# Kernel tuning notes

Measured on AMD Instinct MI355X. Metric: run time of the kernel, lower is better.

Reference implementation:

```python
import jax, jax.numpy as jnp
import numpy as np

BUCKET_SIZE = 64
N_HASHES = 8
EPS = 1e-6
SELF_MASK_VAL = -1e5


def setup_inputs() -> dict:
    key = jax.random.key(0)
    k1, k2, k3 = jax.random.split(key, 3)
    B, S, D = 8, 4096, 128
    n_buckets = S // BUCKET_SIZE  # 64, even as required
    qk = jax.random.normal(k1, (B, S, D), dtype=jnp.float32)
    v = jax.random.normal(k2, (B, S, D), dtype=jnp.float32)
    # shared random rotations (random_rotations_per_head=False): (dim, n_hashes, n_buckets//2)
    rotations = jax.random.normal(k3, (D, N_HASHES, n_buckets // 2), dtype=jnp.float32)
    return {"qk": qk, "v": v, "rotations": rotations}


def _look_one_back(x):
    # prepend previous chunk (with wraparound) along the key/value axis
    x_extra = jnp.concatenate([x[:, -1:], x[:, :-1]], axis=1)
    return jnp.concatenate([x, x_extra], axis=2)


def reference(qk, v, rotations):
    B, S, D = qk.shape
    n_buckets = S // BUCKET_SIZE
    n_bins = n_buckets
    C = N_HASHES * n_bins  # number of chunks per sequence (chunk size = BUCKET_SIZE)

    # --- hash_vectors ---
    rot = jnp.einsum('btf,fhi->bhti', qk, rotations)          # [B,H,S,nb/2]
    rot = jnp.concatenate([rot, -rot], axis=-1)               # [B,H,S,nb]
    buckets = jnp.argmax(rot, axis=-1)                        # [B,H,S]
    offsets = (jnp.arange(N_HASHES) * n_buckets).reshape(1, -1, 1)
    buckets = (buckets + offsets).reshape(B, -1)              # [B, H*S]

    # --- sort tokens by (bucket, position) ---
    ticker = jnp.arange(N_HASHES * S)[None, :]
    buckets_and_t = S * buckets + (ticker % S)                # unique keys
    sticker = jnp.argsort(buckets_and_t, axis=-1)             # [B, H*S]
    undo_sort = jnpp_argsort = jnp.argsort(sticker, axis=-1)
    st = sticker % S

    sqk = jnp.take_along_axis(qk, st[..., None], axis=1)      # [B,H*S,D]
    sv = jnp.take_along_axis(v, st[..., None], axis=1)

    bq_t = st.reshape(B, C, -1)                               # [B,C,chunk]
    bqk = sqk.reshape(B, C, -1, D)
    bv = sv.reshape(B, C, -1, D)

    bq = bqk
    bk = bqk * jax.lax.rsqrt(jnp.sum(bqk * bqk, axis=-1, keepdims=True) + EPS)

    bk = _look_one_back(bk)                                   # [B,C,2*chunk,D]
    bv = _look_one_back(bv)
    bkv_t = _look_one_back(bq_t)

    dots = jnp.einsum('bcie,bcje->bcij', bq, bk) * (D ** -0.5)
    self_mask = bq_t[:, :, :, None] == bkv_t[:, :, None, :]
    dots = jnp.where(self_mask, SELF_MASK_VAL, dots)

    lse = jax.nn.logsumexp(dots, axis=-1, keepdims=True)
    probs = jnp.exp(dots - lse)
    bo = jnp.einsum('bcij,bcje->bcie', probs, bv)             # [B,C,chunk,D]

    so = bo.reshape(B, -1, D)                                 # [B,H*S,D]
    slogits = lse.reshape(B, -1)                              # [B,H*S]

    # unsort
    o = jnp.take_along_axis(so, undo_sort[..., None], axis=1)
    logits = jnp.take_along_axis(slogits, undo_sort, axis=1)

    # combine the n_hashes rounds with softmax over per-round logsumexp
    o = o.reshape(B, N_HASHES, S, D)
    logits = logits.reshape(B, N_HASHES, S, 1)
    w = jnp.exp(logits - jax.nn.logsumexp(logits, axis=1, keepdims=True))
    out = jnp.sum(o * w, axis=1)                              # [B,S,D]
    return out, buckets
```

## Files before the change

### kernel.cpp

```cpp
#include <hip/hip_runtime.h>
#include <hip/hip_bf16.h>

#define BB 8
#define SS 4096
#define DD 128
#define HH 8
#define NBUCK 64
#define CHUNKSZ 64
#define NCHUNK 512
#define HSTOT 32768
#define ROWB 272

typedef __attribute__((ext_vector_type(8))) short short8_t;
typedef __attribute__((ext_vector_type(4))) float f32x4;

static __device__ __forceinline__ unsigned short f2bf(float f) {
    __hip_bfloat16 h = __float2bfloat16(f);
    return *reinterpret_cast<unsigned short*>(&h);
}
static __device__ __forceinline__ unsigned int pk2bf(float lo, float hi) {
    __hip_bfloat162 h = __float22bfloat162_rn(make_float2(lo, hi));
    return *reinterpret_cast<unsigned int*>(&h);
}
static __device__ __forceinline__ float bf2f(unsigned short u) {
    return __uint_as_float(((unsigned int)u) << 16);
}

__global__ __launch_bounds__(256) void hash_kernel(
    const float* __restrict__ qk, const float* __restrict__ rot,
    unsigned char* __restrict__ bucket_ws, float* __restrict__ bucket_out)
{
    const int tid = threadIdx.x;
    const int bid = blockIdx.x;
    const int b   = bid >> 8;
    const int h   = (bid >> 5) & 7;
    const int t0  = (bid & 31) * 128;
    const int tg  = tid >> 3;
    const int jq  = tid & 7;

    const float* qbase = qk + ((size_t)b * SS + t0 + tg * 4) * DD;
    const float* rbase = rot + h * 32 + jq * 4;

    float acc[4][4];
    #pragma unroll
    for (int r = 0; r < 4; ++r)
        #pragma unroll
        for (int j = 0; j < 4; ++j) acc[r][j] = 0.f;

    for (int c = 0; c < 16; ++c) {
        float4 qv[4][2];
        #pragma unroll
        for (int r = 0; r < 4; ++r) {
            qv[r][0] = *reinterpret_cast<const float4*>(qbase + r * DD + c * 8);
            qv[r][1] = *reinterpret_cast<const float4*>(qbase + r * DD + c * 8 + 4);
        }
        float4 rv[8];
        #pragma unroll
        for (int ff = 0; ff < 8; ++ff)
            rv[ff] = *reinterpret_cast<const float4*>(rbase + (size_t)(c * 8 + ff) * (HH * 32));
        #pragma unroll
        for (int ff = 0; ff < 8; ++ff) {
            #pragma unroll
            for (int r = 0; r < 4; ++r) {
                const float4 qh = qv[r][ff >> 2];
                const float qs = (ff & 2) ? ((ff & 1) ? qh.w : qh.z)
                                          : ((ff & 1) ? qh.y : qh.x);
                acc[r][0] = fmaf(qs, rv[ff].x, acc[r][0]);
                acc[r][1] = fmaf(qs, rv[ff].y, acc[r][1]);
                acc[r][2] = fmaf(qs, rv[ff].z, acc[r][2]);
                acc[r][3] = fmaf(qs, rv[ff].w, acc[r][3]);
            }
        }
    }

    const float TAU = 0.01f;
    #pragma unroll
    for (int r = 0; r < 4; ++r) {
        float bv = -3.0e38f; int bi = 0;
        #pragma unroll
        for (int j = 0; j < 4; ++j) {
            float v = acc[r][j];
            if (v > bv) { bv = v; bi = jq * 4 + j; }
        }
        #pragma unroll
        for (int j = 0; j < 4; ++j) {
            float v = -acc[r][j];
            if (v > bv) { bv = v; bi = 32 + jq * 4 + j; }
        }
        #pragma unroll
        for (int off = 1; off < 8; off <<= 1) {
            float ov = __shfl_xor(bv, off);
            int   oi = __shfl_xor(bi, off);
            if (ov > bv || (ov == bv && oi < bi)) { bv = ov; bi = oi; }
        }
        const float thrv = bv - TAU;
        int cnt = 0;
        #pragma unroll
        for (int j = 0; j < 4; ++j) {
            cnt += (acc[r][j]  > thrv) ? 1 : 0;
            cnt += (-acc[r][j] > thrv) ? 1 : 0;
        }
        #pragma unroll
        for (int off = 1; off < 8; off <<= 1) cnt += __shfl_xor(cnt, off);

        const int t = t0 + tg * 4 + r;
        if (cnt > 1) {
            const float* qrow = qk + ((size_t)b * SS + t) * DD;
            double bvd = -1.0e300; int bid2 = 64;
            #pragma unroll
            for (int j = 0; j < 4; ++j) {
                const bool fp = (acc[r][j] > thrv);
                const bool fn = (-acc[r][j] > thrv);
                if (fp || fn) {
                    const float* rcol = rot + h * 32 + jq * 4 + j;
                    double a = 0.0;
                    for (int f = 0; f < DD; ++f)
                        a = fma((double)qrow[f], (double)rcol[(size_t)f * (HH * 32)], a);
                    if (fp &&  a > bvd)                         { bvd = a;  bid2 = jq * 4 + j; }
                    if (fn && (-a > bvd ||
                               (-a == bvd && 32 + jq * 4 + j < bid2))) { bvd = -a; bid2 = 32 + jq * 4 + j; }
                }
            }
            #pragma unroll
            for (int off = 1; off < 8; off <<= 1) {
                double ov = __shfl_xor(bvd, off);
                int    oi = __shfl_xor(bid2, off);
                if (ov > bvd || (ov == bvd && oi < bid2)) { bvd = ov; bid2 = oi; }
            }
            bi = bid2;
        }
        if (jq == 0) {
            const size_t o = ((size_t)b * HH + h) * SS + t;
            bucket_ws[o]  = (unsigned char)bi;
            bucket_out[o] = (float)(bi + h * NBUCK);
        }
    }
}

__global__ __launch_bounds__(256) void sort_kernel(
    const unsigned char* __restrict__ bucket_ws, int* __restrict__ st)
{
    __shared__ unsigned int hist[256 * 65];
    __shared__ unsigned int totals[64];
    const int tid = threadIdx.x;
    const int bh  = blockIdx.x;

    unsigned int* hrow = &hist[tid * 65];
    #pragma unroll
    for (int j = 0; j < 65; ++j) hrow[j] = 0u;

    const uint4 raw = *reinterpret_cast<const uint4*>(bucket_ws + (size_t)bh * SS + tid * 16);
    unsigned int w[4] = {raw.x, raw.y, raw.z, raw.w};

    #pragma unroll
    for (int c = 0; c < 16; ++c) {
        unsigned int bk = (w[c >> 2] >> ((c & 3) * 8)) & 255u;
        hrow[bk] += 1u;
    }
    __syncthreads();

    if (tid < 64) {
        unsigned int run = 0;
        for (int c2 = 0; c2 < 256; ++c2) {
            unsigned int x = hist[c2 * 65 + tid];
            hist[c2 * 65 + tid] = run;
            run += x;
        }
        totals[tid] = run;
    }
    __syncthreads();
    if (tid == 0) {
        unsigned int base = 0;
        for (int k = 0; k < 64; ++k) { unsigned int x = totals[k]; totals[k] = base; base += x; }
    }
    __syncthreads();

    int* dst = st + (size_t)bh * SS;
    #pragma unroll
    for (int c = 0; c < 16; ++c) {
        unsigned int bk = (w[c >> 2] >> ((c & 3) * 8)) & 255u;
        unsigned int pos = totals[bk] + hrow[bk];
        hrow[bk] += 1u;
        dst[pos] = tid * 16 + c;
    }
}

__global__ __launch_bounds__(256, 4) void attn_kernel(
    const float* __restrict__ qk, const float* __restrict__ vv,
    const int* __restrict__ st, float* __restrict__ logits_ws,
    void* __restrict__ o_ws, const int obf16)
{
    __shared__ __align__(16) char smem[36864];
    char*  Kb    = smem;
    char*  Pb    = smem;
    char*  Vt    = smem + 17408;
    int*   tks   = (int*)(smem + 34816);
    float* ninv  = (float*)(smem + 35328);
    float* psums = (float*)(smem + 35840);

    const int tid = threadIdx.x;
    const int bc  = blockIdx.x;
    const int b   = bc >> 9;
    const int c   = bc & 511;
    const int h   = c >> 6;

    if (tid < 128) {
        int src_c = (tid < 64) ? c : ((c == 0) ? (NCHUNK - 1) : (c - 1));
        tks[tid] = st[(size_t)b * HSTOT + (size_t)src_c * CHUNKSZ + (tid & 63)];
    }
    __syncthreads();

    {
        const int row = tid >> 1, half = tid & 1;
        const int t = tks[row];
        const float* srow = qk + ((size_t)b * SS + t) * DD + half * 64;
        char* krow = Kb + (size_t)row * ROWB + half * 128;
        float ss = 0.f;
        #pragma unroll
        for (int i = 0; i < 8; ++i) {
            float4 v0 = *reinterpret_cast<const float4*>(srow + i * 8);
            float4 v1 = *reinterpret_cast<const float4*>(srow + i * 8 + 4);
            ss = fmaf(v0.x, v0.x, ss); ss = fmaf(v0.y, v0.y, ss);
            ss = fmaf(v0.z, v0.z, ss); ss = fmaf(v0.w, v0.w, ss);
            ss = fmaf(v1.x, v1.x, ss); ss = fmaf(v1.y, v1.y, ss);
            ss = fmaf(v1.z, v1.z, ss); ss = fmaf(v1.w, v1.w, ss);
            uint4 pk;
            pk.x = pk2bf(v0.x, v0.y); pk.y = pk2bf(v0.z, v0.w);
            pk.z = pk2bf(v1.x, v1.y); pk.w = pk2bf(v1.z, v1.w);
            *reinterpret_cast<uint4*>(krow + i * 16) = pk;
        }
        psums[tid] = ss;
    }
    __syncthreads();
    if (tid < 128) ninv[tid] = rsqrtf(psums[2 * tid] + psums[2 * tid + 1] + 1e-6f);
    __syncthreads();

    const int w  = tid >> 6;
    const int ln = tid & 63;
    const int cc = ln & 15;
    const int g  = ln >> 4;

    short8_t aq[4];
    #pragma unroll
    for (int ks = 0; ks < 4; ++ks)
        aq[ks] = *reinterpret_cast<const short8_t*>(Kb + (size_t)(16 * w + cc) * ROWB + ks * 64 + g * 16);

    f32x4 acc[8];
    #pragma unroll
    for (int j = 0; j < 8; ++j) {
        acc[j] = (f32x4){0.f, 0.f, 0.f, 0.f};
        #pragma unroll
        for (int ks = 0; ks < 4; ++ks) {
            short8_t bk = *reinterpret_cast<const short8_t*>(Kb + (size_t)(16 * j + cc) * ROWB + ks * 64 + g * 16);
            acc[j] = __builtin_amdgcn_mfma_f32_16x16x32_bf16(aq[ks], bk, acc[j], 0, 0, 0);
        }
    }

    const float SCALE = 0.088388347648318447f;
    float lse[4];
    float pr[8][4];
    #pragma unroll
    for (int jr = 0; jr < 4; ++jr) {
        const int q  = 16 * w + 4 * g + jr;
        const int tq = tks[q];
        float m = -3.0e38f;
        #pragma unroll
        for (int j = 0; j < 8; ++j) {
            const int k = 16 * j + cc;
            float val = acc[j][jr] * (ninv[k] * SCALE);
            if (tks[k] == tq) val = -1e5f;
            pr[j][jr] = val;
            m = fmaxf(m, val);
        }
        #pragma unroll
        for (int off = 1; off < 16; off <<= 1) m = fmaxf(m, __shfl_xor(m, off));
        float ssum = 0.f;
        #pragma unroll
        for (int j = 0; j < 8; ++j) { float ex = expf(pr[j][jr] - m); pr[j][jr] = ex; ssum += ex; }
        #pragma unroll
        for (int off = 1; off < 16; off <<= 1) ssum += __shfl_xor(ssum, off);
        const float inv = 1.0f / ssum;
        #pragma unroll
        for (int j = 0; j < 8; ++j) pr[j][jr] *= inv;
        lse[jr] = m + logf(ssum);
    }

    const int kp = tid & 63;
    const int db = tid >> 6;
    const int tva = tks[2 * kp], tvb = tks[2 * kp + 1];
    const float* vra = vv + ((size_t)b * SS + tva) * DD + db * 16;
    const float* vrb = vv + ((size_t)b * SS + tvb) * DD + db * 16;
    float4 va[4], vbr[4];
    #pragma unroll
    for (int i = 0; i < 4; ++i) {
        va[i]  = *reinterpret_cast<const float4*>(vra + i * 4);
        vbr[i] = *reinterpret_cast<const float4*>(vrb + i * 4);
    }

    __syncthreads();

    #pragma unroll
    for (int jr = 0; jr < 4; ++jr) {
        const int q = 16 * w + 4 * g + jr;
        #pragma unroll
        for (int j = 0; j < 8; ++j)
            *reinterpret_cast<unsigned short*>(Pb + (size_t)q * ROWB + (16 * j + cc) * 2) = f2bf(pr[j][jr]);
    }
    if (cc == 0) {
        #pragma unroll
        for (int jr = 0; jr < 4; ++jr) {
            const int q = 16 * w + 4 * g + jr;
            logits_ws[((size_t)b * HH + h) * SS + tks[q]] = lse[jr];
        }
    }
    {
        const float* fa = reinterpret_cast<const float*>(va);
        const float* fb = reinterpret_cast<const float*>(vbr);
        #pragma unroll
        for (int i = 0; i < 16; ++i) {
            const int dl = db * 16 + i;
            *reinterpret_cast<unsigned int*>(Vt + (size_t)dl * ROWB + kp * 4) = pk2bf(fa[i], fb[i]);
        }
    }
    #pragma unroll
    for (int i = 0; i < 4; ++i) {
        va[i]  = *reinterpret_cast<const float4*>(vra + 64 + i * 4);
        vbr[i] = *reinterpret_cast<const float4*>(vrb + 64 + i * 4);
    }
    __syncthreads();

    short8_t pa[4];
    #pragma unroll
    for (int ks = 0; ks < 4; ++ks)
        pa[ks] = *reinterpret_cast<const short8_t*>(Pb + (size_t)(16 * w + cc) * ROWB + ks * 64 + g * 16);

    f32x4 oacc[8];
    #pragma unroll
    for (int dt = 0; dt < 4; ++dt) {
        oacc[dt] = (f32x4){0.f, 0.f, 0.f, 0.f};
        #pragma unroll
        for (int ks = 0; ks < 4; ++ks) {
            short8_t vb = *reinterpret_cast<const short8_t*>(Vt + (size_t)(16 * dt + cc) * ROWB + ks * 64 + g * 16);
            oacc[dt] = __builtin_amdgcn_mfma_f32_16x16x32_bf16(pa[ks], vb, oacc[dt], 0, 0, 0);
        }
    }
    __syncthreads();

    {
        const float* fa = reinterpret_cast<const float*>(va);
        const float* fb = reinterpret_cast<const float*>(vbr);
        #pragma unroll
        for (int i = 0; i < 16; ++i) {
            const int dl = db * 16 + i;
            *reinterpret_cast<unsigned int*>(Vt + (size_t)dl * ROWB + kp * 4) = pk2bf(fa[i], fb[i]);
        }
    }
    __syncthreads();

    #pragma unroll
    for (int dt = 4; dt < 8; ++dt) {
        oacc[dt] = (f32x4){0.f, 0.f, 0.f, 0.f};
        #pragma unroll
        for (int ks = 0; ks < 4; ++ks) {
            short8_t vb = *reinterpret_cast<const short8_t*>(Vt + (size_t)(16 * (dt - 4) + cc) * ROWB + ks * 64 + g * 16);
            oacc[dt] = __builtin_amdgcn_mfma_f32_16x16x32_bf16(pa[ks], vb, oacc[dt], 0, 0, 0);
        }
    }

    #pragma unroll
    for (int jr = 0; jr < 4; ++jr) {
        const int q = 16 * w + 4 * g + jr;
        const int t = tks[q];
        const size_t base = (((size_t)b * HH + h) * SS + t) * DD + cc;
        if (!obf16) {
            float* op = (float*)o_ws;
            #pragma unroll
            for (int dt = 0; dt < 8; ++dt) op[base + 16 * dt] = oacc[dt][jr];
        } else {
            unsigned short* op = (unsigned short*)o_ws;
            #pragma unroll
            for (int dt = 0; dt < 8; ++dt) op[base + 16 * dt] = f2bf(oacc[dt][jr]);
        }
    }
}

__global__ __launch_bounds__(256) void combine_kernel(
    const float* __restrict__ logits_ws, const void* __restrict__ o_ws,
    float* __restrict__ outp, const int obf16)
{
    const int gid = blockIdx.x * 256 + threadIdx.x;
    const int row = gid >> 5;
    const int seg = gid & 31;
    const int b = row >> 12;
    const int t = row & 4095;

    float l[8];
    float m = -3.0e38f;
    #pragma unroll
    for (int hh = 0; hh < 8; ++hh) {
        l[hh] = logits_ws[((size_t)b * HH + hh) * SS + t];
        m = fmaxf(m, l[hh]);
    }
    float ssum = 0.f;
    #pragma unroll
    for (int hh = 0; hh < 8; ++hh) { l[hh] = expf(l[hh] - m); ssum += l[hh]; }
    const float inv = 1.0f / ssum;

    float a0 = 0.f, a1 = 0.f, a2 = 0.f, a3 = 0.f;
    #pragma unroll
    for (int hh = 0; hh < 8; ++hh) {
        const float wgt = l[hh] * inv;
        const size_t base = (((size_t)b * HH + hh) * SS + t) * DD + seg * 4;
        if (!obf16) {
            float4 ov = *reinterpret_cast<const float4*>((const float*)o_ws + base);
            a0 = fmaf(wgt, ov.x, a0); a1 = fmaf(wgt, ov.y, a1);
            a2 = fmaf(wgt, ov.z, a2); a3 = fmaf(wgt, ov.w, a3);
        } else {
            uint2 u = *reinterpret_cast<const uint2*>((const unsigned short*)o_ws + base);
            a0 = fmaf(wgt, bf2f((unsigned short)(u.x & 0xffffu)), a0);
            a1 = fmaf(wgt, bf2f((unsigned short)(u.x >> 16)), a1);
            a2 = fmaf(wgt, bf2f((unsigned short)(u.y & 0xffffu)), a2);
            a3 = fmaf(wgt, bf2f((unsigned short)(u.y >> 16)), a3);
        }
    }
    *reinterpret_cast<float4*>(outp + ((size_t)b * SS + t) * DD + seg * 4) =
        make_float4(a0, a1, a2, a3);
}

extern "C" void kernel_launch(void* const* d_in, const int* in_sizes, int n_in,
                              void* d_out, int out_size, void* d_ws, size_t ws_size,
                              hipStream_t stream) {
    const float* qk  = (const float*)d_in[0];
    const float* v   = (const float*)d_in[1];
    const float* rot = (const float*)d_in[2];

    float* out        = (float*)d_out;
    float* bucket_out = out + (size_t)BB * SS * DD;

    char* ws = (char*)d_ws;
    int*            st        = (int*)ws;
    unsigned char*  bucket_ws = (unsigned char*)(ws + 1048576);
    float*          logits_ws = (float*)(ws + 1048576 + 262144);
    void*           o_ws      = (void*)(ws + 2359296);

    const int obf16 = 1;

    hipLaunchKernelGGL(hash_kernel,    dim3(2048), dim3(256), 0, stream, qk, rot, bucket_ws, bucket_out);
    hipLaunchKernelGGL(sort_kernel,    dim3(64),   dim3(256), 0, stream, bucket_ws, st);
    hipLaunchKernelGGL(attn_kernel,    dim3(4096), dim3(256), 0, stream, qk, v, st, logits_ws, o_ws, obf16);
    hipLaunchKernelGGL(combine_kernel, dim3(4096), dim3(256), 0, stream, logits_ws, o_ws, out, obf16);
}
```

Before: 190.1 us.

## Compute LSH rotation projections with bf16 MFMA and wider fp64 tie-break fallback

```diff
diff --git a/kernel.cpp b/kernel.cpp
--- a/kernel.cpp
+++ b/kernel.cpp
@@ -13,6 +13,7 @@
 
 typedef __attribute__((ext_vector_type(8))) short short8_t;
 typedef __attribute__((ext_vector_type(4))) float f32x4;
+typedef __attribute__((ext_vector_type(4))) unsigned int u32x4;
 
 static __device__ __forceinline__ unsigned short f2bf(float f) {
     __hip_bfloat16 h = __float2bfloat16(f);
@@ -26,69 +27,89 @@
     return __uint_as_float(((unsigned int)u) << 16);
 }
 
+__global__ __launch_bounds__(256) void rot_transpose_kernel(
+    const float* __restrict__ rot, unsigned short* __restrict__ rotT)
+{
+    const int col = threadIdx.x;
+    for (int f0 = 0; f0 < DD; f0 += 8) {
+        float v[8];
+        #pragma unroll
+        for (int i = 0; i < 8; ++i) v[i] = rot[(size_t)(f0 + i) * 256 + col];
+        uint4 pk;
+        pk.x = pk2bf(v[0], v[1]); pk.y = pk2bf(v[2], v[3]);
+        pk.z = pk2bf(v[4], v[5]); pk.w = pk2bf(v[6], v[7]);
+        *reinterpret_cast<uint4*>(rotT + (size_t)col * DD + f0) = pk;
+    }
+}
+
+__device__ __noinline__ double f64dot_col(const float* __restrict__ qrow,
+                                          const float* __restrict__ rot, int col)
+{
+    double a = 0.0;
+    for (int f = 0; f < DD; ++f)
+        a = fma((double)qrow[f], (double)rot[(size_t)f * 256 + col], a);
+    return a;
+}
+
 __global__ __launch_bounds__(256) void hash_kernel(
     const float* __restrict__ qk, const float* __restrict__ rot,
+    const unsigned short* __restrict__ rotT,
     unsigned char* __restrict__ bucket_ws, float* __restrict__ bucket_out)
 {
     const int tid = threadIdx.x;
     const int bid = blockIdx.x;
-    const int b   = bid >> 8;
-    const int h   = (bid >> 5) & 7;
-    const int t0  = (bid & 31) * 128;
-    const int tg  = tid >> 3;
-    const int jq  = tid & 7;
-
-    const float* qbase = qk + ((size_t)b * SS + t0 + tg * 4) * DD;
-    const float* rbase = rot + h * 32 + jq * 4;
-
-    float acc[4][4];
-    #pragma unroll
-    for (int r = 0; r < 4; ++r)
-        #pragma unroll
-        for (int j = 0; j < 4; ++j) acc[r][j] = 0.f;
-
-    for (int c = 0; c < 16; ++c) {
-        float4 qv[4][2];
-        #pragma unroll
-        for (int r = 0; r < 4; ++r) {
-            qv[r][0] = *reinterpret_cast<const float4*>(qbase + r * DD + c * 8);
-            qv[r][1] = *reinterpret_cast<const float4*>(qbase + r * DD + c * 8 + 4);
-        }
-        float4 rv[8];
-        #pragma unroll
-        for (int ff = 0; ff < 8; ++ff)
-            rv[ff] = *reinterpret_cast<const float4*>(rbase + (size_t)(c * 8 + ff) * (HH * 32));
-        #pragma unroll
-        for (int ff = 0; ff < 8; ++ff) {
+    const int b   = bid >> 6;
+    const int t0  = (bid & 63) * 64;
+    const int w   = tid >> 6;
+    const int ln  = tid & 63;
+    const int cc  = ln & 15;
+    const int g   = ln >> 4;
+    const int tglob = t0 + w * 16 + cc;
+
+    const float* qrow = qk + ((size_t)b * SS + tglob) * DD;
+
+    f32x4 acc[16];
+    #pragma unroll
+    for (int m = 0; m < 16; ++m) acc[m] = (f32x4){0.f, 0.f, 0.f, 0.f};
+
+    #pragma unroll
+    for (int ks = 0; ks < 4; ++ks) {
+        float4 q0 = *reinterpret_cast<const float4*>(qrow + ks * 32 + g * 8);
+        float4 q1 = *reinterpret_cast<const float4*>(qrow + ks * 32 + g * 8 + 4);
+        u32x4 bq;
+        bq.x = pk2bf(q0.x, q0.y); bq.y = pk2bf(q0.z, q0.w);
+        bq.z = pk2bf(q1.x, q1.y); bq.w = pk2bf(q1.z, q1.w);
+        short8_t bfr = __builtin_bit_cast(short8_t, bq);
+        #pragma unroll
+        for (int m = 0; m < 16; ++m) {
+            short8_t af = *reinterpret_cast<const short8_t*>(
+                rotT + (size_t)(16 * m + cc) * DD + ks * 32 + g * 8);
+            acc[m] = __builtin_amdgcn_mfma_f32_16x16x32_bf16(af, bfr, acc[m], 0, 0, 0);
+        }
+    }
+
+    const float TAU = 0.25f;
+    #pragma unroll
+    for (int h = 0; h < 8; ++h) {
+        float bv = -3.0e38f; int bi = 0;
+        #pragma unroll
+        for (int mi = 0; mi < 2; ++mi)
             #pragma unroll
             for (int r = 0; r < 4; ++r) {
-                const float4 qh = qv[r][ff >> 2];
-                const float qs = (ff & 2) ? ((ff & 1) ? qh.w : qh.z)
-                                          : ((ff & 1) ? qh.y : qh.x);
-                acc[r][0] = fmaf(qs, rv[ff].x, acc[r][0]);
-                acc[r][1] = fmaf(qs, rv[ff].y, acc[r][1]);
-                acc[r][2] = fmaf(qs, rv[ff].z, acc[r][2]);
-                acc[r][3] = fmaf(qs, rv[ff].w, acc[r][3]);
+                float v = acc[2 * h + mi][r];
+                int   j = mi * 16 + 4 * g + r;
+                if (v > bv) { bv = v; bi = j; }
             }
-        }
-    }
-
-    const float TAU = 0.01f;
-    #pragma unroll
-    for (int r = 0; r < 4; ++r) {
-        float bv = -3.0e38f; int bi = 0;
-        #pragma unroll
-        for (int j = 0; j < 4; ++j) {
-            float v = acc[r][j];
-            if (v > bv) { bv = v; bi = jq * 4 + j; }
-        }
-        #pragma unroll
-        for (int j = 0; j < 4; ++j) {
-            float v = -acc[r][j];
-            if (v > bv) { bv = v; bi = 32 + jq * 4 + j; }
-        }
-        #pragma unroll
-        for (int off = 1; off < 8; off <<= 1) {
+        #pragma unroll
+        for (int mi = 0; mi < 2; ++mi)
+            #pragma unroll
+            for (int r = 0; r < 4; ++r) {
+                float v = -acc[2 * h + mi][r];
+                int   j = 32 + mi * 16 + 4 * g + r;
+                if (v > bv) { bv = v; bi = j; }
+            }
+        #pragma unroll
+        for (int off = 16; off < 64; off <<= 1) {
             float ov = __shfl_xor(bv, off);
             int   oi = __shfl_xor(bi, off);
             if (ov > bv || (ov == bv && oi < bi)) { bv = ov; bi = oi; }
@@ -96,41 +117,44 @@
         const float thrv = bv - TAU;
         int cnt = 0;
         #pragma unroll
-        for (int j = 0; j < 4; ++j) {
-            cnt += (acc[r][j]  > thrv) ? 1 : 0;
-            cnt += (-acc[r][j] > thrv) ? 1 : 0;
-        }
-        #pragma unroll
-        for (int off = 1; off < 8; off <<= 1) cnt += __shfl_xor(cnt, off);
-
-        const int t = t0 + tg * 4 + r;
+        for (int mi = 0; mi < 2; ++mi)
+            #pragma unroll
+            for (int r = 0; r < 4; ++r) {
+                cnt += (acc[2 * h + mi][r]  > thrv) ? 1 : 0;
+                cnt += (-acc[2 * h + mi][r] > thrv) ? 1 : 0;
+            }
+        #pragma unroll
+        for (int off = 16; off < 64; off <<= 1) cnt += __shfl_xor(cnt, off);
+
         if (cnt > 1) {
-            const float* qrow = qk + ((size_t)b * SS + t) * DD;
+            unsigned int mask = 0;
+            #pragma unroll
+            for (int mi = 0; mi < 2; ++mi)
+                #pragma unroll
+                for (int r = 0; r < 4; ++r) {
+                    if (acc[2 * h + mi][r]  > thrv) mask |= 1u << (mi * 4 + r);
+                    if (-acc[2 * h + mi][r] > thrv) mask |= 1u << (8 + mi * 4 + r);
+                }
             double bvd = -1.0e300; int bid2 = 64;
-            #pragma unroll
-            for (int j = 0; j < 4; ++j) {
-                const bool fp = (acc[r][j] > thrv);
-                const bool fn = (-acc[r][j] > thrv);
-                if (fp || fn) {
-                    const float* rcol = rot + h * 32 + jq * 4 + j;
-                    double a = 0.0;
-                    for (int f = 0; f < DD; ++f)
-                        a = fma((double)qrow[f], (double)rcol[(size_t)f * (HH * 32)], a);
-                    if (fp &&  a > bvd)                         { bvd = a;  bid2 = jq * 4 + j; }
-                    if (fn && (-a > bvd ||
-                               (-a == bvd && 32 + jq * 4 + j < bid2))) { bvd = -a; bid2 = 32 + jq * 4 + j; }
-                }
+            while (mask) {
+                const int s = __ffs(mask) - 1; mask &= mask - 1;
+                const int sign = s >> 3, lr = s & 7, mi = lr >> 2, r = lr & 3;
+                const int j   = mi * 16 + 4 * g + r;
+                const int idx = sign * 32 + j;
+                double a = f64dot_col(qrow, rot, h * 32 + j);
+                double v = sign ? -a : a;
+                if (v > bvd || (v == bvd && idx < bid2)) { bvd = v; bid2 = idx; }
             }
             #pragma unroll
-            for (int off = 1; off < 8; off <<= 1) {
+            for (int off = 16; off < 64; off <<= 1) {
                 double ov = __shfl_xor(bvd, off);
                 int    oi = __shfl_xor(bid2, off);
                 if (ov > bvd || (ov == bvd && oi < bid2)) { bvd = ov; bid2 = oi; }
             }
             bi = bid2;
         }
-        if (jq == 0) {
-            const size_t o = ((size_t)b * HH + h) * SS + t;
+        if (g == 0) {
+            const size_t o = ((size_t)b * HH + h) * SS + tglob;
             bucket_ws[o]  = (unsigned char)bi;
             bucket_out[o] = (float)(bi + h * NBUCK);
         }
@@ -441,11 +465,13 @@
     int*            st        = (int*)ws;
     unsigned char*  bucket_ws = (unsigned char*)(ws + 1048576);
     float*          logits_ws = (float*)(ws + 1048576 + 262144);
-    void*           o_ws      = (void*)(ws + 2359296);
+    unsigned short* rotT      = (unsigned short*)(ws + 2359296);
+    void*           o_ws      = (void*)(ws + 2424832);
 
     const int obf16 = 1;
 
-    hipLaunchKernelGGL(hash_kernel,    dim3(2048), dim3(256), 0, stream, qk, rot, bucket_ws, bucket_out);
+    hipLaunchKernelGGL(rot_transpose_kernel, dim3(1), dim3(256), 0, stream, rot, rotT);
+    hipLaunchKernelGGL(hash_kernel,    dim3(512),  dim3(256), 0, stream, qk, rot, rotT, bucket_ws, bucket_out);
     hipLaunchKernelGGL(sort_kernel,    dim3(64),   dim3(256), 0, stream, bucket_ws, st);
     hipLaunchKernelGGL(attn_kernel,    dim3(4096), dim3(256), 0, stream, qk, v, st, logits_ws, o_ws, obf16);
     hipLaunchKernelGGL(combine_kernel, dim3(4096), dim3(256), 0, stream, logits_ws, o_ws, out, obf16);
```

Measured after the change: 198.6 us. 4.5% more time.
